# Optimization experiments

Hardware: AMD Instinct MI355X
Metric: run time of the kernel (lower is better)

The kernel has to match this reference:

```python
import jax, jax.numpy as jnp
import numpy as np
from jax import lax

B, C, H, WIN, K = 8, 128, 128, 4, 3
WS = H // 2           # window_size = input_resolution / sqrt(win_num)
L = H * H
DN = ('NCHW', 'OIHW', 'NCHW')


def setup_inputs() -> dict:
    key = jax.random.key(0)
    ks = jax.random.split(key, 12)
    s = 0.02
    return {
        'x': jax.random.normal(ks[0], (B, L, C), jnp.float32),
        # ConvLayer1 params: (win_num*dim, dim, k, k), grouped conv, no bias
        'conv1_w': jax.random.normal(ks[1], (WIN * C, C, K, K), jnp.float32) * s,
        'dc_w': jax.random.normal(ks[2], (WIN, C), jnp.float32) * s,
        'dc_b': jax.random.normal(ks[3], (WIN,), jnp.float32) * s,
        'l1_w': jax.random.normal(ks[4], (4 * WIN, WIN), jnp.float32) * s,
        'l1_b': jax.random.normal(ks[5], (4 * WIN,), jnp.float32) * s,
        'l2_w': jax.random.normal(ks[6], (WIN, 4 * WIN), jnp.float32) * s,
        'l2_b': jax.random.normal(ks[7], (WIN,), jnp.float32) * s,
        'gk_w': jax.random.normal(ks[8], (C, WIN, C), jnp.float32) * s,
        'gk_b': jax.random.normal(ks[9], (C,), jnp.float32) * s,
        'fusion_w': jax.random.normal(ks[10], (C, (WIN + 1) * C), jnp.float32) * s,
        'fusion_b': jax.random.normal(ks[11], (C,), jnp.float32) * s,
    }


def reference(x, conv1_w, dc_w, dc_b, l1_w, l1_b, l2_w, l2_b, gk_w, gk_b, fusion_w, fusion_b):
    Bx = x.shape[0]
    # ka_window_partition: (B, L, C) -> (B, win_num*C, WS, WS), window-major channels
    xw = x.reshape(Bx, 2, WS, 2, WS, C).transpose(0, 1, 3, 5, 2, 4).reshape(Bx, WIN * C, WS, WS)
    # convlayer1: grouped conv, groups=win_num
    wc1 = lax.conv_general_dilated(xw, conv1_w, (1, 1), [(1, 1), (1, 1)],
                                   feature_group_count=WIN, dimension_numbers=DN)
    # SE-style window reweighting
    pooled = wc1.mean(axis=(2, 3)).reshape(Bx, WIN, C)          # adaptive avg pool
    ww = jnp.einsum('bwc,wc->bw', pooled, dc_w) + dc_b          # grouped 1x1 downchannel
    ww = jax.nn.gelu(ww @ l1_w.T + l1_b, approximate=False)
    ww = jax.nn.sigmoid(ww @ l2_w.T + l2_b)
    kern = ww[:, :, None, None, None, None] * conv1_w.reshape(WIN, C, C, K, K)[None]
    gk = jnp.einsum('owj,bwijhk->biohk', gk_w, kern) + gk_b[None, None, :, None, None]
    allk = jnp.concatenate([kern, gk[:, None]], axis=1)
    w_all = allk.reshape(Bx * (WIN + 1) * C, C, K, K)
    ximg = x.reshape(Bx, H, H, C).transpose(0, 3, 1, 2)
    xrep = jnp.tile(ximg, (1, WIN + 1, 1, 1)).reshape(1, Bx * (WIN + 1) * C, H, H)
    y = lax.conv_general_dilated(xrep, w_all, (1, 1), [(1, 1), (1, 1)],
                                 feature_group_count=Bx * (WIN + 1), dimension_numbers=DN)
    y = y.reshape(Bx, (WIN + 1) * C, H, H)
    out = jnp.einsum('oc,bchw->bohw', fusion_w, y) + fusion_b[None, :, None, None]
    return out.transpose(0, 2, 3, 1).reshape(Bx, L, C)
```

## Files before the change

kernel.cpp:

```cpp
#include <hip/hip_runtime.h>
#include <hip/hip_bf16.h>
#include <cmath>

typedef unsigned short u16;
typedef __attribute__((ext_vector_type(8))) short bf16x8;
typedef __attribute__((ext_vector_type(4))) float f32x4;
typedef __attribute__((ext_vector_type(4))) unsigned short u16x4;

#define OFF_AGG   0u
#define OFF_WW    81920u
#define OFF_R     82048u
#define OFF_FSUM  100480u
#define OFF_GKT   100992u
#define OFF_A     363136u
#define OFF_P     2722432u
#define OFF_M     5081728u
#define OFF_KEFF  7441024u
#define OFF_XPAD  9800320u

__device__ __forceinline__ u16 f2bf(float f) {
  union { float f; unsigned int u; } v; v.f = f;
  unsigned int r = v.u + 0x7FFFu + ((v.u >> 16) & 1u);
  return (u16)(r >> 16);
}

__global__ void k1_pad_agg(const float* __restrict__ x, u16* __restrict__ xpad,
                           float* __restrict__ agg) {
  const int c = threadIdx.x;
  const int rp = blockIdx.x;
  const int b = blockIdx.y;
  const size_t xpb = ((size_t)b * 130 + rp) * 130 * 128;
  if (rp == 0 || rp == 129) {
    for (int q = 0; q < 130; ++q) xpad[xpb + (size_t)q * 128 + c] = 0;
    return;
  }
  const int r = rp - 1;
  xpad[xpb + c] = 0;
  xpad[xpb + (size_t)129 * 128 + c] = 0;
  const float* xr = x + ((size_t)b * 16384 + (size_t)r * 128) * 128 + c;
  float t0 = 0.f, t1 = 0.f, cF0 = 0.f, cL0 = 0.f, cF1 = 0.f, cL1 = 0.f;
  #pragma unroll 4
  for (int q = 0; q < 128; ++q) {
    float v = xr[(size_t)q * 128];
    xpad[xpb + (size_t)(q + 1) * 128 + c] = f2bf(v);
    if (q < 64) t0 += v; else t1 += v;
    if (q == 0) cF0 = v;
    if (q == 63) cL0 = v;
    if (q == 64) cF1 = v;
    if (q == 127) cL1 = v;
  }
  const int i = r >> 6, rw = r & 63;
  const int a0 = b * 512 + (i * 2) * 128 + c;
  const int a1 = b * 512 + (i * 2 + 1) * 128 + c;
  atomicAdd(&agg[a0], t0);
  atomicAdd(&agg[a1], t1);
  atomicAdd(&agg[3 * 4096 + a0], cF0);
  atomicAdd(&agg[3 * 4096 + a1], cF1);
  atomicAdd(&agg[4 * 4096 + a0], cL0);
  atomicAdd(&agg[4 * 4096 + a1], cL1);
  if (rw == 0)  { atomicAdd(&agg[4096 + a0], t0); atomicAdd(&agg[4096 + a1], t1); }
  if (rw == 63) { atomicAdd(&agg[2 * 4096 + a0], t0); atomicAdd(&agg[2 * 4096 + a1], t1); }
}

__global__ void kR(const float* __restrict__ dc_w, const float* __restrict__ conv1_w,
                   float* __restrict__ R) {
  int gid = blockIdx.x * 256 + threadIdx.x;
  int w = gid / 1152, m = gid % 1152;
  float s = 0.f;
  for (int o = 0; o < 128; ++o)
    s += dc_w[w * 128 + o] * conv1_w[(size_t)(w * 128 + o) * 1152 + m];
  R[gid] = s;
}

__global__ void kT(const float* __restrict__ gk_w, float* __restrict__ gkT) {
  int gid = blockIdx.x * 256 + threadIdx.x;
  int w = gid >> 14, j = (gid >> 7) & 127, c = gid & 127;
  gkT[gid] = gk_w[c * 512 + w * 128 + j];
}

__global__ void kF(const float* __restrict__ fusion_w, float* __restrict__ fsum) {
  int o = threadIdx.x;
  float s = 0.f;
  for (int oc = 0; oc < 128; ++oc) s += fusion_w[o * 640 + 512 + oc];
  fsum[o] = s;
}

__global__ void k2_ww(const float* __restrict__ x, const float* __restrict__ agg,
                      const float* __restrict__ R, const float* __restrict__ dc_b,
                      const float* __restrict__ l1_w, const float* __restrict__ l1_b,
                      const float* __restrict__ l2_w, const float* __restrict__ l2_b,
                      float* __restrict__ ww) {
  const int b = blockIdx.x;
  const int tid = threadIdx.x;
  const int w = tid >> 6, lane = tid & 63;
  __shared__ float red[4];
  float partial = 0.f;
  const int i = w >> 1, j = w & 1;
  const int r0 = i * 64, s0 = j * 64;
  const size_t base = (size_t)b * 16384 * 128;
  #pragma unroll
  for (int k = 0; k < 2; ++k) {
    const int c = lane * 2 + k;
    const int ai = b * 512 + w * 128 + c;
    float T  = agg[ai];
    float rF = agg[4096 + ai];
    float rL = agg[2 * 4096 + ai];
    float cF = agg[3 * 4096 + ai];
    float cL = agg[4 * 4096 + ai];
    float c00 = x[base + ((size_t)(r0 + 0)  * 128 + (s0 + 0))  * 128 + c];
    float c0L = x[base + ((size_t)(r0 + 0)  * 128 + (s0 + 63)) * 128 + c];
    float cL0 = x[base + ((size_t)(r0 + 63) * 128 + (s0 + 0))  * 128 + c];
    float cLL = x[base + ((size_t)(r0 + 63) * 128 + (s0 + 63)) * 128 + c];
    float S[9];
    S[0] = T - rL - cL + cLL;
    S[1] = T - rL;
    S[2] = T - rL - cF + cL0;
    S[3] = T - cL;
    S[4] = T;
    S[5] = T - cF;
    S[6] = T - rF - cL + c0L;
    S[7] = T - rF;
    S[8] = T - rF - cF + c00;
    const float* Rp = R + (w * 128 + c) * 9;
    #pragma unroll
    for (int t = 0; t < 9; ++t) partial += S[t] * Rp[t];
  }
  for (int off = 32; off > 0; off >>= 1) partial += __shfl_xor(partial, off, 64);
  if (lane == 0) red[w] = partial;
  __syncthreads();
  if (tid == 0) {
    float ww0[4];
    #pragma unroll
    for (int w2 = 0; w2 < 4; ++w2) ww0[w2] = red[w2] * (1.f / 4096.f) + dc_b[w2];
    float h1[16];
    for (int i2 = 0; i2 < 16; ++i2) {
      float s = l1_b[i2];
      #pragma unroll
      for (int w2 = 0; w2 < 4; ++w2) s += l1_w[i2 * 4 + w2] * ww0[w2];
      h1[i2] = 0.5f * s * (1.f + erff(s * 0.70710678118654752f));
    }
    for (int w2 = 0; w2 < 4; ++w2) {
      float s = l2_b[w2];
      for (int i2 = 0; i2 < 16; ++i2) s += l2_w[w2 * 16 + i2] * h1[i2];
      ww[b * 4 + w2] = 1.f / (1.f + expf(-s));
    }
  }
}

__global__ void k3_AP(const float* __restrict__ fusion_w, const float* __restrict__ conv1_w,
                      float* __restrict__ A, float* __restrict__ P) {
  int gid = blockIdx.x * 256 + threadIdx.x;
  int w = gid / 36864;
  int rem = gid % 36864;
  int o = rem / 288;
  int m = (rem % 288) * 4;
  const float* fw1 = fusion_w + o * 640 + w * 128;
  const float* fw4 = fusion_w + o * 640 + 512;
  const float* cw = conv1_w + (size_t)w * 128 * 1152 + m;
  float a0 = 0, a1 = 0, a2 = 0, a3 = 0, p0 = 0, p1 = 0, p2 = 0, p3 = 0;
  for (int oc = 0; oc < 128; ++oc) {
    float f1 = fw1[oc], f4 = fw4[oc];
    float4 cv = *(const float4*)(cw + (size_t)oc * 1152);
    a0 += f1 * cv.x; a1 += f1 * cv.y; a2 += f1 * cv.z; a3 += f1 * cv.w;
    p0 += f4 * cv.x; p1 += f4 * cv.y; p2 += f4 * cv.z; p3 += f4 * cv.w;
  }
  float4* Ao = (float4*)(A + (size_t)(w * 128 + o) * 1152 + m);
  float4* Po = (float4*)(P + (size_t)(w * 128 + o) * 1152 + m);
  *Ao = make_float4(a0, a1, a2, a3);
  *Po = make_float4(p0, p1, p2, p3);
}

__global__ void k4_M(const float* __restrict__ A, const float* __restrict__ P,
                     const float* __restrict__ gkT, float* __restrict__ M) {
  int gid = blockIdx.x * 256 + threadIdx.x;
  int w = gid / 36864;
  int rem = gid % 36864;
  int t = rem / 4096;
  int o = (rem % 4096) / 32;
  int c = (rem % 32) * 4;
  const float* Pp = P + (size_t)(w * 128 + o) * 1152 + t;
  const float* Ap = A + (size_t)(w * 128 + o) * 1152 + t;
  const float* g = gkT + w * 16384 + c;
  float acc0 = Ap[(c + 0) * 9], acc1 = Ap[(c + 1) * 9];
  float acc2 = Ap[(c + 2) * 9], acc3 = Ap[(c + 3) * 9];
  for (int j = 0; j < 128; ++j) {
    float pv = Pp[j * 9];
    float4 gv = *(const float4*)(g + j * 128);
    acc0 += pv * gv.x; acc1 += pv * gv.y; acc2 += pv * gv.z; acc3 += pv * gv.w;
  }
  *(float4*)(M + (size_t)((w * 9 + t) * 128 + o) * 128 + c) = make_float4(acc0, acc1, acc2, acc3);
}

__global__ void k5_keff(const float* __restrict__ M, const float* __restrict__ ww,
                        const float* __restrict__ fsum, const float* __restrict__ gk_b,
                        u16* __restrict__ keff) {
  int gid = blockIdx.x * 256 + threadIdx.x;
  int b = gid / 36864;
  int rem = gid % 36864;
  int o = (rem % 4096) / 32;
  int c = (rem % 32) * 4;
  float w0 = ww[b * 4 + 0], w1 = ww[b * 4 + 1], w2 = ww[b * 4 + 2], w3 = ww[b * 4 + 3];
  int mi = rem * 4;
  float4 m0 = *(const float4*)(M + 0 * 147456 + mi);
  float4 m1 = *(const float4*)(M + 1 * 147456 + mi);
  float4 m2 = *(const float4*)(M + 2 * 147456 + mi);
  float4 m3 = *(const float4*)(M + 3 * 147456 + mi);
  float fs = fsum[o];
  float4 gb = *(const float4*)(gk_b + c);
  float r0 = w0 * m0.x + w1 * m1.x + w2 * m2.x + w3 * m3.x + fs * gb.x;
  float r1 = w0 * m0.y + w1 * m1.y + w2 * m2.y + w3 * m3.y + fs * gb.y;
  float r2 = w0 * m0.z + w1 * m1.z + w2 * m2.z + w3 * m3.z + fs * gb.z;
  float r3 = w0 * m0.w + w1 * m1.w + w2 * m2.w + w3 * m3.w + fs * gb.w;
  u16x4 st = { f2bf(r0), f2bf(r1), f2bf(r2), f2bf(r3) };
  *(u16x4*)(keff + (size_t)b * 147456 + mi) = st;
}

__global__ __launch_bounds__(256, 2) void k6_conv(
    const u16* __restrict__ xpad, const u16* __restrict__ keff,
    const float* __restrict__ fusion_b, float* __restrict__ out) {
  __shared__ __align__(16) u16 alds[130 * 128];
  __shared__ __align__(16) u16 apad[256];
  __shared__ __align__(16) u16 wlds[128 * 128];
  const int tid = threadIdx.x;
  const int blk = blockIdx.x;
  const int b = blk & 7;
  const int p = blk >> 3;
  const int wid = tid >> 6;
  const int lane = tid & 63;
  const int wm = (wid & 1) * 64;
  const int wn = (wid >> 1) * 64;
  const int quad = lane >> 4;
  const int l16 = lane & 15;

  f32x4 acc[4][4];
  #pragma unroll
  for (int i = 0; i < 4; ++i)
    #pragma unroll
    for (int j = 0; j < 4; ++j)
      acc[i][j] = (f32x4){0.f, 0.f, 0.f, 0.f};

  const u16* kb = keff + (size_t)b * 147456;
  const u16* xb = xpad + (size_t)b * 130 * 16640;
  bf16x8 streg[8];
  (void)apad;

  auto stage_W_load = [&](int tap) {
    const u16* src = kb + tap * 16384;
    #pragma unroll
    for (int it = 0; it < 8; ++it) {
      const int chunk = it * 256 + tid;
      const int gs = chunk ^ ((chunk >> 4) & 7);
      streg[it] = *(const bf16x8*)(src + gs * 8);
    }
  };
  auto stage_W_write = [&]() {
    #pragma unroll
    for (int it = 0; it < 8; ++it)
      *(bf16x8*)(wlds + (it * 256 + tid) * 8) = streg[it];
  };
  auto stage_A_dma = [&](int prow) {
    const u16* src = xb + (size_t)prow * 16640;
    #pragma unroll
    for (int r = 0; r < 8; ++r) {
      const int chunk = (wid * 8 + r) * 64 + lane;
      const int gs = chunk ^ ((chunk >> 4) & 7);
      __builtin_amdgcn_global_load_lds(
          (const __attribute__((address_space(1))) unsigned int*)(src + (size_t)gs * 8),
          (__attribute__((address_space(3))) unsigned int*)(alds + (wid * 8 + r) * 512),
          16, 0, 0);
    }
    if (tid < 32) {
      const int chunk = 2048 + tid;
      const int gs = chunk ^ ((chunk >> 4) & 7);
      __builtin_amdgcn_global_load_lds(
          (const __attribute__((address_space(1))) unsigned int*)(src + (size_t)gs * 8),
          (__attribute__((address_space(3))) unsigned int*)(alds + 2048 * 8),
          16, 0, 0);
    }
  };

  stage_W_load(0);
  stage_A_dma(p);
  stage_W_write();
  __syncthreads();

  for (int tap = 0; tap < 9; ++tap) {
    if (tap < 8) stage_W_load(tap + 1);
    const int dw = tap % 3 - 1;
    const int pixoff = 1 + dw;
    #pragma unroll
    for (int kc = 0; kc < 4; ++kc) {
      const int c0 = kc * 32 + quad * 8;
      bf16x8 a[4], bb[4];
      #pragma unroll
      for (int i = 0; i < 4; ++i) {
        const int pix = pixoff + wm + i * 16 + l16;
        const int off = (pix * 128 + c0) ^ ((pix & 7) << 3);
        a[i] = *(const bf16x8*)(alds + off);
      }
      #pragma unroll
      for (int j = 0; j < 4; ++j) {
        const int row = wn + j * 16 + l16;
        const int off = (row * 128 + c0) ^ ((row & 7) << 3);
        bb[j] = *(const bf16x8*)(wlds + off);
      }
      #pragma unroll
      for (int i = 0; i < 4; ++i)
        #pragma unroll
        for (int j = 0; j < 4; ++j)
          acc[i][j] = __builtin_amdgcn_mfma_f32_16x16x32_bf16(a[i], bb[j], acc[i][j], 0, 0, 0);
    }
    __syncthreads();
    if (tap < 8) {
      stage_W_write();
      if (tap % 3 == 2) stage_A_dma(p + (tap + 1) / 3);
      __syncthreads();
    }
  }

  float fb[4];
  #pragma unroll
  for (int j = 0; j < 4; ++j) fb[j] = fusion_b[wn + j * 16 + l16];
  float* outb = out + ((size_t)b * 16384 + (size_t)p * 128) * 128;
  #pragma unroll
  for (int i = 0; i < 4; ++i)
    #pragma unroll
    for (int r = 0; r < 4; ++r) {
      const int m = wm + i * 16 + quad * 4 + r;
      #pragma unroll
      for (int j = 0; j < 4; ++j)
        outb[(size_t)m * 128 + (wn + j * 16 + l16)] = acc[i][j][r] + fb[j];
    }
}

extern "C" void kernel_launch(void* const* d_in, const int* in_sizes, int n_in,
                              void* d_out, int out_size, void* d_ws, size_t ws_size,
                              hipStream_t stream) {
  const float* x        = (const float*)d_in[0];
  const float* conv1_w  = (const float*)d_in[1];
  const float* dc_w     = (const float*)d_in[2];
  const float* dc_b     = (const float*)d_in[3];
  const float* l1_w     = (const float*)d_in[4];
  const float* l1_b     = (const float*)d_in[5];
  const float* l2_w     = (const float*)d_in[6];
  const float* l2_b     = (const float*)d_in[7];
  const float* gk_w     = (const float*)d_in[8];
  const float* gk_b     = (const float*)d_in[9];
  const float* fusion_w = (const float*)d_in[10];
  const float* fusion_b = (const float*)d_in[11];
  float* out = (float*)d_out;
  char* ws = (char*)d_ws;

  float* agg  = (float*)(ws + OFF_AGG);
  float* ww   = (float*)(ws + OFF_WW);
  float* R    = (float*)(ws + OFF_R);
  float* fsum = (float*)(ws + OFF_FSUM);
  float* gkT  = (float*)(ws + OFF_GKT);
  float* A    = (float*)(ws + OFF_A);
  float* P    = (float*)(ws + OFF_P);
  float* M    = (float*)(ws + OFF_M);
  u16* keff   = (u16*)(ws + OFF_KEFF);
  u16* xpad   = (u16*)(ws + OFF_XPAD);

  hipMemsetAsync(agg, 0, 81920, stream);
  k1_pad_agg<<<dim3(130, 8), 128, 0, stream>>>(x, xpad, agg);
  kR<<<18, 256, 0, stream>>>(dc_w, conv1_w, R);
  kT<<<256, 256, 0, stream>>>(gk_w, gkT);
  kF<<<1, 128, 0, stream>>>(fusion_w, fsum);
  k2_ww<<<8, 256, 0, stream>>>(x, agg, R, dc_b, l1_w, l1_b, l2_w, l2_b, ww);
  k3_AP<<<576, 256, 0, stream>>>(fusion_w, conv1_w, A, P);
  k4_M<<<576, 256, 0, stream>>>(A, P, gkT, M);
  k5_keff<<<1152, 256, 0, stream>>>(M, ww, fsum, gk_b, keff);
  k6_conv<<<1024, 256, 0, stream>>>(xpad, keff, fusion_b, out);
}
```

Before: 262.9 us.

## Fuse M and keff kernels, merge prep kernels, vectorize pad/aggregate kernel

Merges the three small weight-prep kernels into one launch, and fuses the M computation (P x gkT plus A) with the per-batch keff reweighting so the intermediate M buffer is no longer written and re-read. P and A slices are staged in shared memory and the j-reduction is split across two halves of the block. The pad/aggregate kernel now uses 256 threads with float4 loads, vectorized bf16 stores and a shared-memory reduction, which cuts the number of global atomics. The aim is to reduce launch count and memory traffic in the preprocessing path ahead of the main conv.

```diff
diff --git a/kernel.cpp b/kernel.cpp
--- a/kernel.cpp
+++ b/kernel.cpp
@@ -26,63 +26,97 @@
 
 __global__ void k1_pad_agg(const float* __restrict__ x, u16* __restrict__ xpad,
                            float* __restrict__ agg) {
-  const int c = threadIdx.x;
   const int rp = blockIdx.x;
   const int b = blockIdx.y;
-  const size_t xpb = ((size_t)b * 130 + rp) * 130 * 128;
+  const int tid = threadIdx.x;
+  const size_t xpb = ((size_t)b * 130 + rp) * 16640;
   if (rp == 0 || rp == 129) {
-    for (int q = 0; q < 130; ++q) xpad[xpb + (size_t)q * 128 + c] = 0;
+    const bf16x8 z = {0, 0, 0, 0, 0, 0, 0, 0};
+    #pragma unroll
+    for (int rr = 0; rr < 8; ++rr)
+      *(bf16x8*)(xpad + xpb + (size_t)(rr * 256 + tid) * 8) = z;
+    if (tid < 32)
+      *(bf16x8*)(xpad + xpb + (size_t)(2048 + tid) * 8) = z;
     return;
   }
   const int r = rp - 1;
-  xpad[xpb + c] = 0;
-  xpad[xpb + (size_t)129 * 128 + c] = 0;
-  const float* xr = x + ((size_t)b * 16384 + (size_t)r * 128) * 128 + c;
-  float t0 = 0.f, t1 = 0.f, cF0 = 0.f, cL0 = 0.f, cF1 = 0.f, cL1 = 0.f;
-  #pragma unroll 4
-  for (int q = 0; q < 128; ++q) {
-    float v = xr[(size_t)q * 128];
-    xpad[xpb + (size_t)(q + 1) * 128 + c] = f2bf(v);
-    if (q < 64) t0 += v; else t1 += v;
-    if (q == 0) cF0 = v;
-    if (q == 63) cL0 = v;
-    if (q == 64) cF1 = v;
-    if (q == 127) cL1 = v;
+  if (tid < 32) {
+    *(u16x4*)(xpad + xpb + tid * 4) = (u16x4){0, 0, 0, 0};
+  } else if (tid < 64) {
+    *(u16x4*)(xpad + xpb + 129 * 128 + (tid - 32) * 4) = (u16x4){0, 0, 0, 0};
+  }
+  const int s = tid >> 5;
+  const int cg = tid & 31;
+  const int c0 = cg * 4;
+  const float* xr = x + ((size_t)b * 16384 + (size_t)r * 128) * 128;
+  f32x4 sum = {0.f, 0.f, 0.f, 0.f};
+  f32x4 cap = {0.f, 0.f, 0.f, 0.f};
+  #pragma unroll
+  for (int qi = 0; qi < 16; ++qi) {
+    const int q = s * 16 + qi;
+    f32x4 v = *(const f32x4*)(xr + (size_t)q * 128 + c0);
+    sum += v;
+    if (qi == 0 && (s == 0 || s == 4)) cap = v;
+    if (qi == 15 && (s == 3 || s == 7)) cap = v;
+    u16x4 st = { f2bf(v[0]), f2bf(v[1]), f2bf(v[2]), f2bf(v[3]) };
+    *(u16x4*)(xpad + xpb + (size_t)(q + 1) * 128 + c0) = st;
   }
   const int i = r >> 6, rw = r & 63;
-  const int a0 = b * 512 + (i * 2) * 128 + c;
-  const int a1 = b * 512 + (i * 2 + 1) * 128 + c;
-  atomicAdd(&agg[a0], t0);
-  atomicAdd(&agg[a1], t1);
-  atomicAdd(&agg[3 * 4096 + a0], cF0);
-  atomicAdd(&agg[3 * 4096 + a1], cF1);
-  atomicAdd(&agg[4 * 4096 + a0], cL0);
-  atomicAdd(&agg[4 * 4096 + a1], cL1);
-  if (rw == 0)  { atomicAdd(&agg[4096 + a0], t0); atomicAdd(&agg[4096 + a1], t1); }
-  if (rw == 63) { atomicAdd(&agg[2 * 4096 + a0], t0); atomicAdd(&agg[2 * 4096 + a1], t1); }
-}
-
-__global__ void kR(const float* __restrict__ dc_w, const float* __restrict__ conv1_w,
-                   float* __restrict__ R) {
-  int gid = blockIdx.x * 256 + threadIdx.x;
-  int w = gid / 1152, m = gid % 1152;
-  float s = 0.f;
-  for (int o = 0; o < 128; ++o)
-    s += dc_w[w * 128 + o] * conv1_w[(size_t)(w * 128 + o) * 1152 + m];
-  R[gid] = s;
-}
-
-__global__ void kT(const float* __restrict__ gk_w, float* __restrict__ gkT) {
-  int gid = blockIdx.x * 256 + threadIdx.x;
-  int w = gid >> 14, j = (gid >> 7) & 127, c = gid & 127;
-  gkT[gid] = gk_w[c * 512 + w * 128 + j];
-}
-
-__global__ void kF(const float* __restrict__ fusion_w, float* __restrict__ fsum) {
-  int o = threadIdx.x;
-  float s = 0.f;
-  for (int oc = 0; oc < 128; ++oc) s += fusion_w[o * 640 + 512 + oc];
-  fsum[o] = s;
+  const int abase = b * 512 + c0;
+  if (s == 0) {
+    #pragma unroll
+    for (int k = 0; k < 4; ++k) atomicAdd(&agg[3 * 4096 + abase + (i * 2) * 128 + k], cap[k]);
+  } else if (s == 4) {
+    #pragma unroll
+    for (int k = 0; k < 4; ++k) atomicAdd(&agg[3 * 4096 + abase + (i * 2 + 1) * 128 + k], cap[k]);
+  } else if (s == 3) {
+    #pragma unroll
+    for (int k = 0; k < 4; ++k) atomicAdd(&agg[4 * 4096 + abase + (i * 2) * 128 + k], cap[k]);
+  } else if (s == 7) {
+    #pragma unroll
+    for (int k = 0; k < 4; ++k) atomicAdd(&agg[4 * 4096 + abase + (i * 2 + 1) * 128 + k], cap[k]);
+  }
+  __shared__ f32x4 ls[8][32];
+  ls[s][cg] = sum;
+  __syncthreads();
+  if (tid < 64) {
+    const int h = tid >> 5, g = tid & 31;
+    f32x4 T = ls[h * 4 + 0][g] + ls[h * 4 + 1][g] + ls[h * 4 + 2][g] + ls[h * 4 + 3][g];
+    const int a = b * 512 + (i * 2 + h) * 128 + g * 4;
+    #pragma unroll
+    for (int k = 0; k < 4; ++k) atomicAdd(&agg[a + k], T[k]);
+    if (rw == 0) {
+      #pragma unroll
+      for (int k = 0; k < 4; ++k) atomicAdd(&agg[4096 + a + k], T[k]);
+    }
+    if (rw == 63) {
+      #pragma unroll
+      for (int k = 0; k < 4; ++k) atomicAdd(&agg[2 * 4096 + a + k], T[k]);
+    }
+  }
+}
+
+__global__ void kprep(const float* __restrict__ dc_w, const float* __restrict__ conv1_w,
+                      const float* __restrict__ gk_w, const float* __restrict__ fusion_w,
+                      float* __restrict__ R, float* __restrict__ gkT,
+                      float* __restrict__ fsum) {
+  const int bid = blockIdx.x, tid = threadIdx.x;
+  if (bid < 18) {
+    int gid = bid * 256 + tid;
+    int w = gid / 1152, m = gid % 1152;
+    float s = 0.f;
+    for (int o = 0; o < 128; ++o)
+      s += dc_w[w * 128 + o] * conv1_w[(size_t)(w * 128 + o) * 1152 + m];
+    R[gid] = s;
+  } else if (bid < 274) {
+    int gid = (bid - 18) * 256 + tid;
+    int w = gid >> 14, j = (gid >> 7) & 127, c = gid & 127;
+    gkT[gid] = gk_w[c * 512 + w * 128 + j];
+  } else if (tid < 128) {
+    float s = 0.f;
+    for (int oc = 0; oc < 128; ++oc) s += fusion_w[tid * 640 + 512 + oc];
+    fsum[tid] = s;
+  }
 }
 
 __global__ void k2_ww(const float* __restrict__ x, const float* __restrict__ agg,
@@ -170,49 +204,64 @@
   *Po = make_float4(p0, p1, p2, p3);
 }
 
-__global__ void k4_M(const float* __restrict__ A, const float* __restrict__ P,
-                     const float* __restrict__ gkT, float* __restrict__ M) {
-  int gid = blockIdx.x * 256 + threadIdx.x;
-  int w = gid / 36864;
-  int rem = gid % 36864;
-  int t = rem / 4096;
-  int o = (rem % 4096) / 32;
-  int c = (rem % 32) * 4;
-  const float* Pp = P + (size_t)(w * 128 + o) * 1152 + t;
-  const float* Ap = A + (size_t)(w * 128 + o) * 1152 + t;
-  const float* g = gkT + w * 16384 + c;
-  float acc0 = Ap[(c + 0) * 9], acc1 = Ap[(c + 1) * 9];
-  float acc2 = Ap[(c + 2) * 9], acc3 = Ap[(c + 3) * 9];
-  for (int j = 0; j < 128; ++j) {
-    float pv = Pp[j * 9];
-    float4 gv = *(const float4*)(g + j * 128);
-    acc0 += pv * gv.x; acc1 += pv * gv.y; acc2 += pv * gv.z; acc3 += pv * gv.w;
-  }
-  *(float4*)(M + (size_t)((w * 9 + t) * 128 + o) * 128 + c) = make_float4(acc0, acc1, acc2, acc3);
-}
-
-__global__ void k5_keff(const float* __restrict__ M, const float* __restrict__ ww,
-                        const float* __restrict__ fsum, const float* __restrict__ gk_b,
-                        u16* __restrict__ keff) {
-  int gid = blockIdx.x * 256 + threadIdx.x;
-  int b = gid / 36864;
-  int rem = gid % 36864;
-  int o = (rem % 4096) / 32;
-  int c = (rem % 32) * 4;
-  float w0 = ww[b * 4 + 0], w1 = ww[b * 4 + 1], w2 = ww[b * 4 + 2], w3 = ww[b * 4 + 3];
-  int mi = rem * 4;
-  float4 m0 = *(const float4*)(M + 0 * 147456 + mi);
-  float4 m1 = *(const float4*)(M + 1 * 147456 + mi);
-  float4 m2 = *(const float4*)(M + 2 * 147456 + mi);
-  float4 m3 = *(const float4*)(M + 3 * 147456 + mi);
-  float fs = fsum[o];
-  float4 gb = *(const float4*)(gk_b + c);
-  float r0 = w0 * m0.x + w1 * m1.x + w2 * m2.x + w3 * m3.x + fs * gb.x;
-  float r1 = w0 * m0.y + w1 * m1.y + w2 * m2.y + w3 * m3.y + fs * gb.y;
-  float r2 = w0 * m0.z + w1 * m1.z + w2 * m2.z + w3 * m3.z + fs * gb.z;
-  float r3 = w0 * m0.w + w1 * m1.w + w2 * m2.w + w3 * m3.w + fs * gb.w;
-  u16x4 st = { f2bf(r0), f2bf(r1), f2bf(r2), f2bf(r3) };
-  *(u16x4*)(keff + (size_t)b * 147456 + mi) = st;
+__global__ void k45_keff(const float* __restrict__ A, const float* __restrict__ P,
+                         const float* __restrict__ gkT, const float* __restrict__ ww,
+                         const float* __restrict__ fsum, const float* __restrict__ gk_b,
+                         u16* __restrict__ keff) {
+  const int t = blockIdx.x >> 6;
+  const int o0 = (blockIdx.x & 63) * 2;
+  const int tid = threadIdx.x;
+  __shared__ float pl[2][4][128];
+  __shared__ float al[2][4][128];
+  __shared__ float red[2][2][4][128];
+  #pragma unroll
+  for (int rr = 0; rr < 4; ++rr) {
+    const int idx = rr * 256 + tid;
+    const int oi = idx >> 9, w = (idx >> 7) & 3, j = idx & 127;
+    const size_t src = (size_t)(w * 128 + o0 + oi) * 1152 + j * 9 + t;
+    pl[oi][w][j] = P[src];
+    al[oi][w][j] = A[src];
+  }
+  __syncthreads();
+  const int c = tid & 127, jh = tid >> 7;
+  float acc[2][4];
+  #pragma unroll
+  for (int oi = 0; oi < 2; ++oi)
+    #pragma unroll
+    for (int w = 0; w < 4; ++w) acc[oi][w] = 0.f;
+  const float* g = gkT + c;
+  #pragma unroll 4
+  for (int j = jh * 64; j < jh * 64 + 64; ++j) {
+    const float g0 = g[0 * 16384 + j * 128];
+    const float g1 = g[1 * 16384 + j * 128];
+    const float g2 = g[2 * 16384 + j * 128];
+    const float g3 = g[3 * 16384 + j * 128];
+    #pragma unroll
+    for (int oi = 0; oi < 2; ++oi) {
+      acc[oi][0] += pl[oi][0][j] * g0;
+      acc[oi][1] += pl[oi][1][j] * g1;
+      acc[oi][2] += pl[oi][2][j] * g2;
+      acc[oi][3] += pl[oi][3][j] * g3;
+    }
+  }
+  #pragma unroll
+  for (int oi = 0; oi < 2; ++oi)
+    #pragma unroll
+    for (int w = 0; w < 4; ++w) red[jh][oi][w][c] = acc[oi][w];
+  __syncthreads();
+  const int oi2 = tid >> 7, c2 = tid & 127;
+  float m[4];
+  #pragma unroll
+  for (int w = 0; w < 4; ++w)
+    m[w] = red[0][oi2][w][c2] + red[1][oi2][w][c2] + al[oi2][w][c2];
+  const float base = fsum[o0 + oi2] * gk_b[c2];
+  #pragma unroll
+  for (int b = 0; b < 8; ++b) {
+    float r = base;
+    #pragma unroll
+    for (int w = 0; w < 4; ++w) r += ww[b * 4 + w] * m[w];
+    keff[(size_t)b * 147456 + (size_t)t * 16384 + (o0 + oi2) * 128 + c2] = f2bf(r);
+  }
 }
 
 __global__ __launch_bounds__(256, 2) void k6_conv(
@@ -358,18 +407,14 @@
   float* gkT  = (float*)(ws + OFF_GKT);
   float* A    = (float*)(ws + OFF_A);
   float* P    = (float*)(ws + OFF_P);
-  float* M    = (float*)(ws + OFF_M);
   u16* keff   = (u16*)(ws + OFF_KEFF);
   u16* xpad   = (u16*)(ws + OFF_XPAD);
 
   hipMemsetAsync(agg, 0, 81920, stream);
-  k1_pad_agg<<<dim3(130, 8), 128, 0, stream>>>(x, xpad, agg);
-  kR<<<18, 256, 0, stream>>>(dc_w, conv1_w, R);
-  kT<<<256, 256, 0, stream>>>(gk_w, gkT);
-  kF<<<1, 128, 0, stream>>>(fusion_w, fsum);
+  k1_pad_agg<<<dim3(130, 8), 256, 0, stream>>>(x, xpad, agg);
+  kprep<<<275, 256, 0, stream>>>(dc_w, conv1_w, gk_w, fusion_w, R, gkT, fsum);
   k2_ww<<<8, 256, 0, stream>>>(x, agg, R, dc_b, l1_w, l1_b, l2_w, l2_b, ww);
   k3_AP<<<576, 256, 0, stream>>>(fusion_w, conv1_w, A, P);
-  k4_M<<<576, 256, 0, stream>>>(A, P, gkT, M);
-  k5_keff<<<1152, 256, 0, stream>>>(M, ww, fsum, gk_b, keff);
+  k45_keff<<<576, 256, 0, stream>>>(A, P, gkT, ww, fsum, gk_b, keff);
   k6_conv<<<1024, 256, 0, stream>>>(xpad, keff, fusion_b, out);
 }
```

Measured after the change: 246.1 us. 1.07x faster.
